# Optimization experiments

Hardware: AMD Instinct MI355X
Metric: run time of the kernel (lower is better)

## Reference

```python
import jax, jax.numpy as jnp
import numpy as np

B, S, D, H = 4, 2048, 1024, 16
HD = D // H
DFF = 4 * D
EPS = 1e-5


def setup_inputs() -> dict:
    key = jax.random.key(0)
    ks = jax.random.split(key, 8)
    s = 0.02
    return {
        "x": jax.random.normal(ks[0], (B, S, D), dtype=jnp.float32),
        "ln1_g": jnp.ones((D,), jnp.float32),
        "ln1_b": jnp.zeros((D,), jnp.float32),
        "Wq": jax.random.normal(ks[1], (D, D), jnp.float32) * s,
        "Wk": jax.random.normal(ks[2], (D, D), jnp.float32) * s,
        "Wv": jax.random.normal(ks[3], (D, D), jnp.float32) * s,
        "Wo": jax.random.normal(ks[4], (D, D), jnp.float32) * s,
        "ln2_g": jnp.ones((D,), jnp.float32),
        "ln2_b": jnp.zeros((D,), jnp.float32),
        "W1": jax.random.normal(ks[5], (D, DFF), jnp.float32) * s,
        "b1": jnp.zeros((DFF,), jnp.float32),
        "W2": jax.random.normal(ks[6], (DFF, D), jnp.float32) * s,
        "b2": jnp.zeros((D,), jnp.float32),
    }


def _layernorm(x, g, b):
    mu = jnp.mean(x, axis=-1, keepdims=True)
    var = jnp.var(x, axis=-1, keepdims=True)
    return (x - mu) * jax.lax.rsqrt(var + EPS) * g + b


def _block(x, ln1_g, ln1_b, Wq, Wk, Wv, Wo, ln2_g, ln2_b, W1, b1, W2, b2):
    # --- attention sub-block (pre-norm) ---
    h = _layernorm(x, ln1_g, ln1_b)
    q = (h @ Wq).reshape(B, S, H, HD)
    k = (h @ Wk).reshape(B, S, H, HD)
    v = (h @ Wv).reshape(B, S, H, HD)
    scores = jnp.einsum("bqhd,bkhd->bhqk", q, k) / np.sqrt(HD).astype(np.float32)
    causal = jnp.tril(jnp.ones((S, S), dtype=bool))
    scores = jnp.where(causal, scores, -jnp.inf)
    attn = jax.nn.softmax(scores, axis=-1)  # dropout p=0 (eval)
    ctx = jnp.einsum("bhqk,bkhd->bqhd", attn, v).reshape(B, S, D)
    x = x + ctx @ Wo
    # --- FFN sub-block (pre-norm) ---
    h = _layernorm(x, ln2_g, ln2_b)
    h = jax.nn.gelu(h @ W1 + b1, approximate=False)  # torch nn.GELU() = exact erf
    return x + (h @ W2 + b2)


def reference(x, ln1_g, ln1_b, Wq, Wk, Wv, Wo, ln2_g, ln2_b, W1, b1, W2, b2):
    return _block(x, ln1_g, ln1_b, Wq, Wk, Wv, Wo, ln2_g, ln2_b, W1, b1, W2, b2)
```

## Files before the change

### kernel.cpp

```cpp
#include <hip/hip_runtime.h>
#include <hip/hip_bf16.h>
#include <math.h>

#define NB 4
#define NS 2048
#define ND 1024
#define NH 16
#define NHD 64
#define NDFF 4096
#define QKS 3072

typedef __attribute__((ext_vector_type(8))) short bf16x8;
typedef __attribute__((ext_vector_type(4))) float f32x4;
typedef __attribute__((ext_vector_type(16))) float f32x16;
typedef __attribute__((ext_vector_type(4))) short short4v;
typedef __attribute__((ext_vector_type(4))) int i32x4;

static __device__ __forceinline__ short f2b(float f) {
  union { __hip_bfloat16 b; short s; } u;
  u.b = __float2bfloat16(f);
  return u.s;
}
static __device__ __forceinline__ float b2f(short s) {
  union { float f; unsigned u; } v;
  v.u = ((unsigned)(unsigned short)s) << 16;
  return v.f;
}

static __device__ __forceinline__ int cvtpk(float lo, float hi_) {
  int r;
  asm("v_cvt_pk_bf16_f32 %0, %1, %2" : "=v"(r) : "v"(lo), "v"(hi_));
  return r;
}

static __device__ __forceinline__ float pairsum(float x) {
  auto r = __builtin_amdgcn_permlane32_swap(__float_as_uint(x), __float_as_uint(x), false, false);
  return __uint_as_float(r[0]) + __uint_as_float(r[1]);
}

static __device__ __forceinline__ float gelu_t(float v) {
  const float u = v * (0.7978845608f + 0.0356774081f * v * v);
  return v / (1.0f + __expf(-2.0f * u));
}

template <bool BF16IN>
__global__ __launch_bounds__(256) void ln_kernel(
    const void* __restrict__ xin, const float* __restrict__ g,
    const float* __restrict__ b, short* __restrict__ out) {
  __shared__ float red[8];
  const int row = blockIdx.x;
  const int t = threadIdx.x;
  float xv[4];
  if (BF16IN) {
    const short4v sv = *(const short4v*)((const short*)xin + (size_t)row * ND + t * 4);
#pragma unroll
    for (int i = 0; i < 4; ++i) xv[i] = b2f(sv[i]);
  } else {
    const float4 fv = *(const float4*)((const float*)xin + (size_t)row * ND + t * 4);
    xv[0] = fv.x; xv[1] = fv.y; xv[2] = fv.z; xv[3] = fv.w;
  }
  float s = xv[0] + xv[1] + xv[2] + xv[3];
  float ss = xv[0] * xv[0] + xv[1] * xv[1] + xv[2] * xv[2] + xv[3] * xv[3];
#pragma unroll
  for (int m = 32; m >= 1; m >>= 1) {
    s += __shfl_xor(s, m);
    ss += __shfl_xor(ss, m);
  }
  if ((t & 63) == 0) { red[(t >> 6) * 2] = s; red[(t >> 6) * 2 + 1] = ss; }
  __syncthreads();
  s = red[0] + red[2] + red[4] + red[6];
  ss = red[1] + red[3] + red[5] + red[7];
  const float mu = s * (1.0f / ND);
  const float var = ss * (1.0f / ND) - mu * mu;
  const float rs = rsqrtf(var + 1e-5f);
  const float4 gv = *(const float4*)(g + t * 4);
  const float4 bv = *(const float4*)(b + t * 4);
  short o[4];
  o[0] = f2b((xv[0] - mu) * rs * gv.x + bv.x);
  o[1] = f2b((xv[1] - mu) * rs * gv.y + bv.y);
  o[2] = f2b((xv[2] - mu) * rs * gv.z + bv.z);
  o[3] = f2b((xv[3] - mu) * rs * gv.w + bv.w);
  *(short4v*)(out + (size_t)row * ND + t * 4) = *(short4v*)o;
}

__global__ __launch_bounds__(256) void tcast_kernel(
    const float* __restrict__ in, short* __restrict__ out, int K, int N) {
  __shared__ float tile[32][33];
  const int n0 = blockIdx.x * 32, k0 = blockIdx.y * 32;
  const int tx = threadIdx.x & 31, ty = threadIdx.x >> 5;
#pragma unroll
  for (int i = 0; i < 32; i += 8)
    tile[ty + i][tx] = in[(size_t)(k0 + ty + i) * N + n0 + tx];
  __syncthreads();
#pragma unroll
  for (int i = 0; i < 32; i += 8)
    out[(size_t)(n0 + ty + i) * K + k0 + tx] = f2b(tile[tx][ty + i]);
}

__global__ __launch_bounds__(256) void tcast4_kernel(
    const float* __restrict__ w0, const float* __restrict__ w1,
    const float* __restrict__ w2, const float* __restrict__ w3,
    short* __restrict__ dqkv, short* __restrict__ dwo) {
  __shared__ float tile[32][33];
  const int z = blockIdx.z;
  const float* in = (z == 0) ? w0 : (z == 1) ? w1 : (z == 2) ? w2 : w3;
  short* out = (z < 3) ? dqkv + (size_t)z * 1024 * 1024 : dwo;
  const int n0 = blockIdx.x * 32, k0 = blockIdx.y * 32;
  const int tx = threadIdx.x & 31, ty = threadIdx.x >> 5;
#pragma unroll
  for (int i = 0; i < 32; i += 8)
    tile[ty + i][tx] = in[(size_t)(k0 + ty + i) * 1024 + n0 + tx];
  __syncthreads();
#pragma unroll
  for (int i = 0; i < 32; i += 8)
    out[(size_t)(n0 + ty + i) * 1024 + k0 + tx] = f2b(tile[tx][ty + i]);
}

__global__ __launch_bounds__(256) void vtrans_kernel(
    const short* __restrict__ in, short* __restrict__ out) {
  __shared__ short tile[64][72];
  const int s0 = blockIdx.x * 64, bh = blockIdx.y;
  const int bb = bh >> 4, hh = bh & 15;
  const int rr = threadIdx.x >> 3, cc = (threadIdx.x & 7) * 8;
#pragma unroll
  for (int it = 0; it < 2; ++it) {
    const int r = rr + it * 32;
    *(bf16x8*)&tile[r][cc] =
        *(const bf16x8*)&in[((size_t)(bb * NS + s0 + r)) * QKS + 2048 + hh * NHD + cc];
  }
  __syncthreads();
  const size_t ob = (size_t)bh * NHD * NS;
#pragma unroll
  for (int it = 0; it < 2; ++it) {
    const int d = rr + it * 32;
    short o[8];
#pragma unroll
    for (int j = 0; j < 8; ++j) o[j] = tile[cc + j][d];
    *(bf16x8*)&out[ob + (size_t)d * NS + s0 + cc] = *(bf16x8*)o;
  }
}

__device__ __forceinline__ void gload16(const void* g, void* l) {
  __builtin_amdgcn_global_load_lds(
      (const __attribute__((address_space(1))) unsigned int*)g,
      (__attribute__((address_space(3))) unsigned int*)l, 16, 0, 0);
}

template <int GM, int GN, int EPI>
__global__ __launch_bounds__(256, 3) void gemms_kernel(
    const short* __restrict__ A, const short* __restrict__ Bt,
    float* __restrict__ Cf, short* __restrict__ Cb,
    const float* __restrict__ bias, const float* __restrict__ resf,
    const short* __restrict__ resb, int M, int N, int K) {
  __shared__ short lds[2 * 128 * 64];
  const int tid = threadIdx.x, l = tid & 63, w = tid >> 6;
  const int wm = w >> 1, wn = w & 1;
  const int nbm = M >> 7, nbn = N >> 7, nwg = nbm * nbn;
  int wg = blockIdx.x;
  wg = (wg & 7) * (nwg >> 3) + (wg >> 3);
  const int gidx = wg / (GM * GN), r = wg % (GM * GN);
  const int ngn = nbn / GN;
  const int bm = (gidx / ngn) * GM + r / GN;
  const int bn = (gidx % ngn) * GN + r % GN;

  const int srow = tid >> 3;
  const int sslot = (tid & 7) ^ (srow & 7);
  const short* Asrc = A + (size_t)(bm * 128 + srow) * K + sslot * 8;
  const short* Bsrc = Bt + (size_t)(bn * 128 + srow) * K + sslot * 8;
  const int wdst = w * 512;

  const int fr = l & 15, fg4 = l >> 4;
  int arow[4], brow[4];
#pragma unroll
  for (int i = 0; i < 4; ++i) {
    arow[i] = wm * 64 + i * 16 + fr;
    brow[i] = wn * 64 + i * 16 + fr;
  }

  f32x4 acc[4][4] = {};
  const int NT = K >> 6;

#pragma unroll
  for (int j = 0; j < 4; ++j) {
    gload16(Asrc, &lds[j * 2048 + wdst]);
    gload16(Bsrc, &lds[8192 + j * 2048 + wdst]);
    Asrc += (size_t)32 * K;
    Bsrc += (size_t)32 * K;
  }
  Asrc -= (size_t)128 * K;
  Bsrc -= (size_t)128 * K;

  for (int t = 0; t < NT; ++t) {
    __syncthreads();
#pragma unroll
    for (int kh = 0; kh < 2; ++kh) {
      bf16x8 af[4], bf[4];
#pragma unroll
      for (int i = 0; i < 4; ++i) {
        af[i] = *(const bf16x8*)&lds[arow[i] * 64 + (((kh * 4 + fg4) ^ (arow[i] & 7)) << 3)];
        bf[i] = *(const bf16x8*)&lds[8192 + brow[i] * 64 + (((kh * 4 + fg4) ^ (brow[i] & 7)) << 3)];
      }
      __builtin_amdgcn_s_setprio(1);
#pragma unroll
      for (int mi = 0; mi < 4; ++mi)
#pragma unroll
        for (int ni = 0; ni < 4; ++ni)
          acc[mi][ni] = __builtin_amdgcn_mfma_f32_16x16x32_bf16(bf[ni], af[mi], acc[mi][ni], 0, 0, 0);
      __builtin_amdgcn_s_setprio(0);
    }
    __syncthreads();
    if (t + 1 < NT) {
      const short* a = Asrc + (size_t)(t + 1) * 64;
      const short* b = Bsrc + (size_t)(t + 1) * 64;
#pragma unroll
      for (int j = 0; j < 4; ++j) {
        gload16(a, &lds[j * 2048 + wdst]);
        gload16(b, &lds[8192 + j * 2048 + wdst]);
        a += (size_t)32 * K;
        b += (size_t)32 * K;
      }
    }
  }

  const int fq = fg4 * 4;
  const int wrb = bm * 128 + wm * 64;
  const int wcb = bn * 128 + wn * 64;
#pragma unroll
  for (int mi = 0; mi < 4; ++mi) {
    const int row = wrb + mi * 16 + fr;
#pragma unroll
    for (int ni = 0; ni < 4; ++ni) {
      const int col = wcb + ni * 16 + fq;
      const f32x4 v = acc[mi][ni];
      if (EPI == 0) {
        short o[4];
#pragma unroll
        for (int rr = 0; rr < 4; ++rr) o[rr] = f2b(v[rr]);
        *(short4v*)&Cb[(size_t)row * N + col] = *(short4v*)o;
      } else if (EPI == 1) {
        const f32x4 rv = *(const f32x4*)&resf[(size_t)row * N + col];
        short o[4];
#pragma unroll
        for (int rr = 0; rr < 4; ++rr) o[rr] = f2b(v[rr] + rv[rr]);
        *(short4v*)&Cb[(size_t)row * N + col] = *(short4v*)o;
      } else if (EPI == 2) {
        const f32x4 bv = *(const f32x4*)&bias[col];
        short o[4];
#pragma unroll
        for (int rr = 0; rr < 4; ++rr) o[rr] = f2b(gelu_t(v[rr] + bv[rr]));
        *(short4v*)&Cb[(size_t)row * N + col] = *(short4v*)o;
      } else {
        const f32x4 bv = *(const f32x4*)&bias[col];
        const short4v rv = *(const short4v*)&resb[(size_t)row * N + col];
        f32x4 o;
#pragma unroll
        for (int rr = 0; rr < 4; ++rr) o[rr] = v[rr] + bv[rr] + b2f(rv[rr]);
        *(f32x4*)&Cf[(size_t)row * N + col] = o;
      }
    }
  }
}

__global__ __launch_bounds__(256, 2) void attn_kernel(
    const short* __restrict__ qkv, const short* __restrict__ vt, short* __restrict__ ctx) {
  __shared__ short Kls[2][64 * 64];
  __shared__ short Vls[2][64 * 64];

  const int bid = blockIdx.x;
  const int bh = (bid & 7) * 8 + ((bid >> 3) & 7);
  const int cp = bid >> 6;
  const int bb = bh >> 4, hh = bh & 15;
  const int lane = threadIdx.x & 63, wave = threadIdx.x >> 6;
  const int ql = lane & 31, hi = lane >> 5;
  const int qbA = cp * 128 + wave * 32;
  const int qbB = (15 - cp) * 128 + wave * 32;

  bf16x8 qf[2][4];
#pragma unroll
  for (int hf = 0; hf < 2; ++hf) {
    const int qb0 = hf ? qbB : qbA;
    const size_t qrow = ((size_t)bb * NS + qb0 + ql) * QKS + hh * NHD;
#pragma unroll
    for (int st = 0; st < 4; ++st)
      qf[hf][st] = *(const bf16x8*)&qkv[qrow + st * 16 + hi * 8];
  }

  f32x16 acc[2][2] = {};
  float l_run[2] = {0.f, 0.f};

  const int srow = lane >> 3;
  const int sslot = (lane & 7) ^ srow;
  const short* kbasep = qkv + (size_t)bb * NS * QKS + 1024 + hh * NHD + sslot * 8;
  const short* vbasep = vt + (size_t)bh * NHD * NS + sslot * 8;

  const int nkt = (16 - cp) * 2;
#pragma unroll
  for (int r = 0; r < 2; ++r) {
    const int row = r * 32 + wave * 8 + srow;
    gload16(kbasep + (size_t)row * QKS, &Kls[0][(r * 32 + wave * 8) * 64]);
    gload16(vbasep + (size_t)row * NS, &Vls[0][(r * 32 + wave * 8) * 64]);
  }

  int buf = 0;
  for (int jt = 0; jt < nkt; ++jt) {
    asm volatile("s_waitcnt vmcnt(0) lgkmcnt(0)\n\ts_barrier" ::: "memory");
    if (jt + 1 < nkt) {
      const int k0n = (jt + 1) * 64;
#pragma unroll
      for (int r = 0; r < 2; ++r) {
        const int row = r * 32 + wave * 8 + srow;
        gload16(kbasep + (size_t)(k0n + row) * QKS, &Kls[buf ^ 1][(r * 32 + wave * 8) * 64]);
        gload16(vbasep + (size_t)row * NS + k0n, &Vls[buf ^ 1][(r * 32 + wave * 8) * 64]);
      }
    }
    const int k0 = jt * 64;
    const short* Kb = &Kls[buf][0];
    const short* Vb = &Vls[buf][0];
#pragma unroll
    for (int ks = 0; ks < 2; ++ks) {
      const int kbase = k0 + ks * 32;
      if (kbase > qbB) continue;
      bf16x8 kf[4], vf[2][2];
      const int krow = ks * 32 + ql;
#pragma unroll
      for (int st = 0; st < 4; ++st)
        kf[st] = *(const bf16x8*)&Kb[krow * 64 + ((st * 2 + hi) ^ (krow & 7)) * 8];
#pragma unroll
      for (int db = 0; db < 2; ++db) {
        const int vrow = db * 32 + ql;
#pragma unroll
        for (int su = 0; su < 2; ++su)
          vf[db][su] =
              *(const bf16x8*)&Vb[vrow * 64 + ((ks * 4 + su * 2 + hi) ^ (vrow & 7)) * 8];
      }
#pragma unroll
      for (int hf = 0; hf < 2; ++hf) {
        const int qb0 = hf ? qbB : qbA;
        if (kbase > qb0) continue;
        const int qg = qb0 + ql;
        f32x16 s = {};
        __builtin_amdgcn_s_setprio(1);
#pragma unroll
        for (int st = 0; st < 4; ++st)
          s = __builtin_amdgcn_mfma_f32_32x32x16_bf16(kf[st], qf[hf][st], s, 0, 0, 0);
        __builtin_amdgcn_s_setprio(0);
        const bool masked = (kbase + 31 > qb0);
        float pe[16];
        float lt = 0.f;
#pragma unroll
        for (int r = 0; r < 16; ++r) {
          float sv = s[r];
          if (masked) {
            const int key = kbase + 4 * hi + (r & 3) + 8 * (r >> 2);
            sv = (key > qg) ? -1e38f : sv;
          }
          pe[r] = exp2f(sv * 0.18033688011112042f);
          lt += pe[r];
        }
        l_run[hf] += pairsum(lt);
        bf16x8 pf[2];
#pragma unroll
        for (int su = 0; su < 2; ++su) {
          const int a0 = cvtpk(pe[su * 8 + 0], pe[su * 8 + 1]);
          const int a1 = cvtpk(pe[su * 8 + 2], pe[su * 8 + 3]);
          const int b0 = cvtpk(pe[su * 8 + 4], pe[su * 8 + 5]);
          const int b1 = cvtpk(pe[su * 8 + 6], pe[su * 8 + 7]);
          auto r0 = __builtin_amdgcn_permlane32_swap((unsigned)a0, (unsigned)b0, false, false);
          auto r1 = __builtin_amdgcn_permlane32_swap((unsigned)a1, (unsigned)b1, false, false);
          union { i32x4 w; bf16x8 v; } u;
          u.w[0] = r0[0]; u.w[1] = r1[0]; u.w[2] = r0[1]; u.w[3] = r1[1];
          pf[su] = u.v;
        }
        __builtin_amdgcn_s_setprio(1);
#pragma unroll
        for (int su = 0; su < 2; ++su) {
          acc[hf][0] = __builtin_amdgcn_mfma_f32_32x32x16_bf16(vf[0][su], pf[su], acc[hf][0], 0, 0, 0);
          acc[hf][1] = __builtin_amdgcn_mfma_f32_32x32x16_bf16(vf[1][su], pf[su], acc[hf][1], 0, 0, 0);
        }
        __builtin_amdgcn_s_setprio(0);
      }
    }
    buf ^= 1;
  }

#pragma unroll
  for (int hf = 0; hf < 2; ++hf) {
    const int qb0 = hf ? qbB : qbA;
    const float inv = 1.0f / l_run[hf];
    const size_t ob = ((size_t)bb * NS + qb0 + ql) * ND + hh * NHD + hi * 8;
#pragma unroll
    for (int db = 0; db < 2; ++db) {
#pragma unroll
      for (int J = 0; J < 2; ++J) {
        const int a0 = cvtpk(acc[hf][db][J * 8 + 0] * inv, acc[hf][db][J * 8 + 1] * inv);
        const int a1 = cvtpk(acc[hf][db][J * 8 + 2] * inv, acc[hf][db][J * 8 + 3] * inv);
        const int b0 = cvtpk(acc[hf][db][J * 8 + 4] * inv, acc[hf][db][J * 8 + 5] * inv);
        const int b1 = cvtpk(acc[hf][db][J * 8 + 6] * inv, acc[hf][db][J * 8 + 7] * inv);
        auto r0 = __builtin_amdgcn_permlane32_swap((unsigned)a0, (unsigned)b0, false, false);
        auto r1 = __builtin_amdgcn_permlane32_swap((unsigned)a1, (unsigned)b1, false, false);
        union { i32x4 w; bf16x8 v; } u;
        u.w[0] = r0[0]; u.w[1] = r1[0]; u.w[2] = r0[1]; u.w[3] = r1[1];
        *(bf16x8*)&ctx[ob + db * 32 + J * 16] = u.v;
      }
    }
  }
}

extern "C" void kernel_launch(void* const* d_in, const int* in_sizes, int n_in,
                              void* d_out, int out_size, void* d_ws, size_t ws_size,
                              hipStream_t stream) {
  (void)in_sizes; (void)n_in; (void)out_size; (void)ws_size;
  const float* x     = (const float*)d_in[0];
  const float* ln1_g = (const float*)d_in[1];
  const float* ln1_b = (const float*)d_in[2];
  const float* Wq    = (const float*)d_in[3];
  const float* Wk    = (const float*)d_in[4];
  const float* Wv    = (const float*)d_in[5];
  const float* Wo    = (const float*)d_in[6];
  const float* ln2_g = (const float*)d_in[7];
  const float* ln2_b = (const float*)d_in[8];
  const float* W1    = (const float*)d_in[9];
  const float* b1    = (const float*)d_in[10];
  const float* W2    = (const float*)d_in[11];
  const float* b2    = (const float*)d_in[12];
  float* out = (float*)d_out;

  char* ws = (char*)d_ws;
  const size_t MiB = 1024 * 1024;
  short* wqkvT = (short*)(ws + 0 * MiB);
  short* woT   = (short*)(ws + 6 * MiB);
  short* w1T   = (short*)(ws + 8 * MiB);
  short* w2T   = (short*)(ws + 16 * MiB);
  short* h     = (short*)(ws + 24 * MiB);
  short* ctx   = (short*)(ws + 24 * MiB);
  short* qkv   = (short*)(ws + 40 * MiB);
  short* vt    = (short*)(ws + 88 * MiB);
  short* hff   = (short*)(ws + 40 * MiB);
  short* x1b   = (short*)(ws + 104 * MiB);

  tcast4_kernel<<<dim3(32, 32, 4), 256, 0, stream>>>(Wq, Wk, Wv, Wo, wqkvT, woT);
  tcast_kernel<<<dim3(128, 32), 256, 0, stream>>>(W1, w1T, 1024, 4096);
  tcast_kernel<<<dim3(32, 128), 256, 0, stream>>>(W2, w2T, 4096, 1024);

  ln_kernel<false><<<8192, 256, 0, stream>>>(x, ln1_g, ln1_b, h);

  gemms_kernel<4, 6, 0><<<1536, 256, 0, stream>>>(h, wqkvT, nullptr, qkv, nullptr,
                                                  nullptr, nullptr, 8192, 3072, 1024);
  vtrans_kernel<<<dim3(32, 64), 256, 0, stream>>>(qkv, vt);

  attn_kernel<<<512, 256, 0, stream>>>(qkv, vt, ctx);

  gemms_kernel<4, 8, 1><<<512, 256, 0, stream>>>(ctx, woT, nullptr, x1b, nullptr,
                                                 x, nullptr, 8192, 1024, 1024);

  ln_kernel<true><<<8192, 256, 0, stream>>>(x1b, ln2_g, ln2_b, h);

  gemms_kernel<4, 8, 2><<<2048, 256, 0, stream>>>(h, w1T, nullptr, hff, b1,
                                                  nullptr, nullptr, 8192, 4096, 1024);
  gemms_kernel<2, 2, 3><<<512, 256, 0, stream>>>(hff, w2T, out, nullptr, b2,
                                                 nullptr, x1b, 8192, 1024, 4096);
}
```

Baseline: 353.4 us.

## Split paired causal query chunks into separate attention blocks, heaviest first

The attention kernel previously gave each block two query chunks (cp and 15-cp) so causal work was balanced per block. Now each block handles one 128-row query chunk, the grid doubles to 1024 blocks, and chunks are issued heaviest-first (ch = 15 - bid>>6) for dynamic load balancing. Registers per thread drop (one accumulator set instead of two), and launch bounds are raised to 4 blocks per CU for higher occupancy. The cost is that K/V tiles are now loaded separately by each single-chunk block instead of being shared across the two paired chunks, which increases memory traffic.

```diff
diff --git a/kernel.cpp b/kernel.cpp
--- a/kernel.cpp
+++ b/kernel.cpp
@@ -261,39 +261,36 @@
   }
 }
 
-__global__ __launch_bounds__(256, 2) void attn_kernel(
+__global__ __launch_bounds__(256, 4) void attn_kernel(
     const short* __restrict__ qkv, const short* __restrict__ vt, short* __restrict__ ctx) {
   __shared__ short Kls[2][64 * 64];
   __shared__ short Vls[2][64 * 64];
 
   const int bid = blockIdx.x;
   const int bh = (bid & 7) * 8 + ((bid >> 3) & 7);
-  const int cp = bid >> 6;
+  const int ch = 15 - (bid >> 6);
   const int bb = bh >> 4, hh = bh & 15;
   const int lane = threadIdx.x & 63, wave = threadIdx.x >> 6;
   const int ql = lane & 31, hi = lane >> 5;
-  const int qbA = cp * 128 + wave * 32;
-  const int qbB = (15 - cp) * 128 + wave * 32;
-
-  bf16x8 qf[2][4];
-#pragma unroll
-  for (int hf = 0; hf < 2; ++hf) {
-    const int qb0 = hf ? qbB : qbA;
+  const int qb0 = ch * 128 + wave * 32;
+
+  bf16x8 qf[4];
+  {
     const size_t qrow = ((size_t)bb * NS + qb0 + ql) * QKS + hh * NHD;
 #pragma unroll
     for (int st = 0; st < 4; ++st)
-      qf[hf][st] = *(const bf16x8*)&qkv[qrow + st * 16 + hi * 8];
-  }
-
-  f32x16 acc[2][2] = {};
-  float l_run[2] = {0.f, 0.f};
+      qf[st] = *(const bf16x8*)&qkv[qrow + st * 16 + hi * 8];
+  }
+
+  f32x16 acc[2] = {};
+  float l_run = 0.f;
 
   const int srow = lane >> 3;
   const int sslot = (lane & 7) ^ srow;
   const short* kbasep = qkv + (size_t)bb * NS * QKS + 1024 + hh * NHD + sslot * 8;
   const short* vbasep = vt + (size_t)bh * NHD * NS + sslot * 8;
 
-  const int nkt = (16 - cp) * 2;
+  const int nkt = (ch + 1) * 2;
 #pragma unroll
   for (int r = 0; r < 2; ++r) {
     const int row = r * 32 + wave * 8 + srow;
@@ -319,7 +316,7 @@
 #pragma unroll
     for (int ks = 0; ks < 2; ++ks) {
       const int kbase = k0 + ks * 32;
-      if (kbase > qbB) continue;
+      if (kbase > qb0) continue;
       bf16x8 kf[4], vf[2][2];
       const int krow = ks * 32 + ql;
 #pragma unroll
@@ -333,69 +330,62 @@
           vf[db][su] =
               *(const bf16x8*)&Vb[vrow * 64 + ((ks * 4 + su * 2 + hi) ^ (vrow & 7)) * 8];
       }
-#pragma unroll
-      for (int hf = 0; hf < 2; ++hf) {
-        const int qb0 = hf ? qbB : qbA;
-        if (kbase > qb0) continue;
-        const int qg = qb0 + ql;
-        f32x16 s = {};
-        __builtin_amdgcn_s_setprio(1);
-#pragma unroll
-        for (int st = 0; st < 4; ++st)
-          s = __builtin_amdgcn_mfma_f32_32x32x16_bf16(kf[st], qf[hf][st], s, 0, 0, 0);
-        __builtin_amdgcn_s_setprio(0);
-        const bool masked = (kbase + 31 > qb0);
-        float pe[16];
-        float lt = 0.f;
-#pragma unroll
-        for (int r = 0; r < 16; ++r) {
-          float sv = s[r];
-          if (masked) {
-            const int key = kbase + 4 * hi + (r & 3) + 8 * (r >> 2);
-            sv = (key > qg) ? -1e38f : sv;
-          }
-          pe[r] = exp2f(sv * 0.18033688011112042f);
-          lt += pe[r];
+      const int qg = qb0 + ql;
+      f32x16 s = {};
+      __builtin_amdgcn_s_setprio(1);
+#pragma unroll
+      for (int st = 0; st < 4; ++st)
+        s = __builtin_amdgcn_mfma_f32_32x32x16_bf16(kf[st], qf[st], s, 0, 0, 0);
+      __builtin_amdgcn_s_setprio(0);
+      const bool masked = (kbase + 31 > qb0);
+      float pe[16];
+      float lt = 0.f;
+#pragma unroll
+      for (int r = 0; r < 16; ++r) {
+        float sv = s[r];
+        if (masked) {
+          const int key = kbase + 4 * hi + (r & 3) + 8 * (r >> 2);
+          sv = (key > qg) ? -1e38f : sv;
         }
-        l_run[hf] += pairsum(lt);
-        bf16x8 pf[2];
-#pragma unroll
-        for (int su = 0; su < 2; ++su) {
-          const int a0 = cvtpk(pe[su * 8 + 0], pe[su * 8 + 1]);
-          const int a1 = cvtpk(pe[su * 8 + 2], pe[su * 8 + 3]);
-          const int b0 = cvtpk(pe[su * 8 + 4], pe[su * 8 + 5]);
-          const int b1 = cvtpk(pe[su * 8 + 6], pe[su * 8 + 7]);
-          auto r0 = __builtin_amdgcn_permlane32_swap((unsigned)a0, (unsigned)b0, false, false);
-          auto r1 = __builtin_amdgcn_permlane32_swap((unsigned)a1, (unsigned)b1, false, false);
-          union { i32x4 w; bf16x8 v; } u;
-          u.w[0] = r0[0]; u.w[1] = r1[0]; u.w[2] = r0[1]; u.w[3] = r1[1];
-          pf[su] = u.v;
-        }
-        __builtin_amdgcn_s_setprio(1);
-#pragma unroll
-        for (int su = 0; su < 2; ++su) {
-          acc[hf][0] = __builtin_amdgcn_mfma_f32_32x32x16_bf16(vf[0][su], pf[su], acc[hf][0], 0, 0, 0);
-          acc[hf][1] = __builtin_amdgcn_mfma_f32_32x32x16_bf16(vf[1][su], pf[su], acc[hf][1], 0, 0, 0);
-        }
-        __builtin_amdgcn_s_setprio(0);
-      }
+        pe[r] = exp2f(sv * 0.18033688011112042f);
+        lt += pe[r];
+      }
+      l_run += pairsum(lt);
+      bf16x8 pf[2];
+#pragma unroll
+      for (int su = 0; su < 2; ++su) {
+        const int a0 = cvtpk(pe[su * 8 + 0], pe[su * 8 + 1]);
+        const int a1 = cvtpk(pe[su * 8 + 2], pe[su * 8 + 3]);
+        const int b0 = cvtpk(pe[su * 8 + 4], pe[su * 8 + 5]);
+        const int b1 = cvtpk(pe[su * 8 + 6], pe[su * 8 + 7]);
+        auto r0 = __builtin_amdgcn_permlane32_swap((unsigned)a0, (unsigned)b0, false, false);
+        auto r1 = __builtin_amdgcn_permlane32_swap((unsigned)a1, (unsigned)b1, false, false);
+        union { i32x4 w; bf16x8 v; } u;
+        u.w[0] = r0[0]; u.w[1] = r1[0]; u.w[2] = r0[1]; u.w[3] = r1[1];
+        pf[su] = u.v;
+      }
+      __builtin_amdgcn_s_setprio(1);
+#pragma unroll
+      for (int su = 0; su < 2; ++su) {
+        acc[0] = __builtin_amdgcn_mfma_f32_32x32x16_bf16(vf[0][su], pf[su], acc[0], 0, 0, 0);
+        acc[1] = __builtin_amdgcn_mfma_f32_32x32x16_bf16(vf[1][su], pf[su], acc[1], 0, 0, 0);
+      }
+      __builtin_amdgcn_s_setprio(0);
     }
     buf ^= 1;
   }
 
-#pragma unroll
-  for (int hf = 0; hf < 2; ++hf) {
-    const int qb0 = hf ? qbB : qbA;
-    const float inv = 1.0f / l_run[hf];
+  {
+    const float inv = 1.0f / l_run;
     const size_t ob = ((size_t)bb * NS + qb0 + ql) * ND + hh * NHD + hi * 8;
 #pragma unroll
     for (int db = 0; db < 2; ++db) {
 #pragma unroll
       for (int J = 0; J < 2; ++J) {
-        const int a0 = cvtpk(acc[hf][db][J * 8 + 0] * inv, acc[hf][db][J * 8 + 1] * inv);
-        const int a1 = cvtpk(acc[hf][db][J * 8 + 2] * inv, acc[hf][db][J * 8 + 3] * inv);
-        const int b0 = cvtpk(acc[hf][db][J * 8 + 4] * inv, acc[hf][db][J * 8 + 5] * inv);
-        const int b1 = cvtpk(acc[hf][db][J * 8 + 6] * inv, acc[hf][db][J * 8 + 7] * inv);
+        const int a0 = cvtpk(acc[db][J * 8 + 0] * inv, acc[db][J * 8 + 1] * inv);
+        const int a1 = cvtpk(acc[db][J * 8 + 2] * inv, acc[db][J * 8 + 3] * inv);
+        const int b0 = cvtpk(acc[db][J * 8 + 4] * inv, acc[db][J * 8 + 5] * inv);
+        const int b1 = cvtpk(acc[db][J * 8 + 6] * inv, acc[db][J * 8 + 7] * inv);
         auto r0 = __builtin_amdgcn_permlane32_swap((unsigned)a0, (unsigned)b0, false, false);
         auto r1 = __builtin_amdgcn_permlane32_swap((unsigned)a1, (unsigned)b1, false, false);
         union { i32x4 w; bf16x8 v; } u;
@@ -448,7 +438,7 @@
                                                   nullptr, nullptr, 8192, 3072, 1024);
   vtrans_kernel<<<dim3(32, 64), 256, 0, stream>>>(qkv, vt);
 
-  attn_kernel<<<512, 256, 0, stream>>>(qkv, vt, ctx);
+  attn_kernel<<<1024, 256, 0, stream>>>(qkv, vt, ctx);
 
   gemms_kernel<4, 8, 1><<<512, 256, 0, stream>>>(ctx, woT, nullptr, x1b, nullptr,
                                                  x, nullptr, 8192, 1024, 1024);
```

After: 347.4 us. No clear change (-1.7%).
